# Kernel tuning notes

Measured on AMD Instinct MI355X. Metric: run time of the kernel, lower is better.

Reference implementation:

```python
import jax, jax.numpy as jnp
import numpy as np

BATCH = 16384
IN = 1024
OUT = 1024
SIGMA_MIN = 0.1
SIGMA_MAX = 1.0


def setup_inputs() -> dict:
    key = jax.random.key(0)
    k0, k1, k2, k3 = jax.random.split(key, 4)
    x = jax.random.normal(k0, (BATCH, IN), dtype=jnp.float32)
    # torch init: triu(randn) -> upper-triangular reflector banks
    U = jnp.triu(jax.random.normal(k1, (IN, IN), dtype=jnp.float32))
    V = jnp.triu(jax.random.normal(k2, (OUT, OUT), dtype=jnp.float32))
    p = 0.001 * jax.random.normal(k3, (min(IN, OUT),), dtype=jnp.float32)
    bias = jnp.zeros((OUT,), dtype=jnp.float32)
    return {"x": x, "U": U, "V": V, "p": p, "bias": bias}


def _hprod_step(x, u):
    # u has zeros in its first i entries (triu row i), so the full-vector
    # form equals torch's sliced Hprod on the last k = n - i columns.
    alpha = 2.0 * (x @ u) / jnp.dot(u, u)          # [bs]
    return x - alpha[:, None] * u[None, :], None   # rank-1 update


def reference(x, U, V, p, bias):
    r = (SIGMA_MAX - SIGMA_MIN) / 2.0
    sigma_mean = SIGMA_MIN + r
    # mask enforces torch slice semantics (entries below diag never used)
    Um = U * jnp.triu(jnp.ones_like(U))
    Vm = V * jnp.triu(jnp.ones_like(V))
    # Umultiply: reflectors i = 0 .. n_U-1 in order (sequential recurrence)
    x, _ = jax.lax.scan(_hprod_step, x, Um)
    # Sigma: diagonal scaling (square case IN == OUT)
    sigmas = 2.0 * r * (jax.nn.sigmoid(p) - 0.5) + sigma_mean
    x = x * sigmas[None, :]
    # Vmultiply: reflectors i = n_V-1 .. 0 (reverse order)
    x, _ = jax.lax.scan(_hprod_step, x, Vm[::-1])
    return x + bias
```

## Files before the change

kernel.cpp:

```cpp
#include <hip/hip_runtime.h>
#include <stdint.h>

typedef __attribute__((ext_vector_type(8))) short short8;
typedef __attribute__((ext_vector_type(4))) float f32x4;

#define NN 1024
#define NBATCH 16384
#define ME ((size_t)NN * NN)
#define AS1 (const __attribute__((address_space(1))) void*)
#define AS3 (__attribute__((address_space(3))) void*)

__device__ __forceinline__ unsigned short f32_to_bf16_rne(float f) {
  unsigned int u = __float_as_uint(f);
  unsigned int r = (u + 0x7fffu + ((u >> 16) & 1u)) >> 16;
  return (unsigned short)r;
}

__device__ __forceinline__ unsigned int pack2bf(float lo, float hi) {
  return (unsigned int)f32_to_bf16_rne(lo) | ((unsigned int)f32_to_bf16_rne(hi) << 16);
}

__device__ __forceinline__ void split_bf16(float x, unsigned short& h, unsigned short& l) {
  h = f32_to_bf16_rne(x);
  float hf = __uint_as_float((unsigned int)h << 16);
  l = f32_to_bf16_rne(x - hf);
}

__device__ __forceinline__ float allsum64(float x) {
  x += __int_as_float(__builtin_amdgcn_update_dpp(0, __float_as_int(x), 0xB1, 0xF, 0xF, true));
  x += __int_as_float(__builtin_amdgcn_update_dpp(0, __float_as_int(x), 0x4E, 0xF, 0xF, true));
  x += __int_as_float(__builtin_amdgcn_update_dpp(0, __float_as_int(x), 0x141, 0xF, 0xF, true));
  x += __int_as_float(__builtin_amdgcn_update_dpp(0, __float_as_int(x), 0x140, 0xF, 0xF, true));
#if __has_builtin(__builtin_amdgcn_permlane16_swap) && __has_builtin(__builtin_amdgcn_permlane32_swap)
  {
    auto r16 = __builtin_amdgcn_permlane16_swap(__float_as_uint(x), __float_as_uint(x), false, false);
    x = __uint_as_float(r16[0]) + __uint_as_float(r16[1]);
    auto r32 = __builtin_amdgcn_permlane32_swap(__float_as_uint(x), __float_as_uint(x), false, false);
    x = __uint_as_float(r32[0]) + __uint_as_float(r32[1]);
  }
#else
  x += __int_as_float(__builtin_amdgcn_ds_swizzle(__float_as_int(x), 0x401F));
  x += __shfl_xor(x, 32);
#endif
  return x;
}

__global__ __launch_bounds__(256) void prep_kernel(
    const float* __restrict__ U, const float* __restrict__ V,
    const float* __restrict__ p, float* __restrict__ tau_u,
    float* __restrict__ tau_v, float* __restrict__ sigmas) {
  int wave = threadIdx.x >> 6, lane = threadIdx.x & 63;
  int row = blockIdx.x * 4 + wave;
  if (row < 2048) {
    const float* u = (row < NN) ? (U + (size_t)row * NN) : (V + (size_t)(row - NN) * NN);
    float s = 0.f;
#pragma unroll
    for (int t = 0; t < 16; ++t) { float a = u[lane + (t << 6)]; s += a * a; }
    s = allsum64(s);
    if (lane == 0) {
      float tau = 2.0f / s;
      if (row < NN) tau_u[row] = tau;
      else tau_v[row - NN] = tau;
    }
  } else if (row < 2064) {
    int j = ((row - 2048) << 6) + lane;
    float pj = p[j];
    float sg = 1.0f / (1.0f + expf(-pj));
    sigmas[j] = 0.9f * (sg - 0.5f) + 0.55f;
  }
}

__global__ __launch_bounds__(256) void castx_kernel(
    const float* __restrict__ X, unsigned short* __restrict__ Xb) {
  const size_t n4 = (size_t)NBATCH * NN / 4;
  for (size_t i = (size_t)blockIdx.x * 256 + threadIdx.x; i < n4; i += (size_t)gridDim.x * 256) {
    float4 v = reinterpret_cast<const float4*>(X)[i];
    uint2 o;
    o.x = pack2bf(v.x, v.y);
    o.y = pack2bf(v.z, v.w);
    reinterpret_cast<uint2*>(Xb)[i] = o;
  }
}

__global__ __launch_bounds__(64) void gram_t8_kernel(
    const float* __restrict__ U, const float* __restrict__ V,
    const float* __restrict__ tau_u, const float* __restrict__ tau_v,
    float* __restrict__ T8all) {
  __shared__ float G[64];
  const int blk = blockIdx.x;
  const int lane = threadIdx.x;
  const float* bank;
  int rbase, rsign, st;
  if (blk < 128) { bank = U; rbase = 8 * blk; rsign = 1; st = 8 * blk; }
  else { int s = blk - 128; bank = V; rbase = 1023 - 8 * s; rsign = -1; st = 1016 - 8 * s; }

  if (lane < 28) {
    int j = 1, k = 0, t = lane;
    for (int jj = 1; jj < 8; ++jj) {
      int lo = jj * (jj - 1) / 2, hi = jj * (jj + 1) / 2;
      if (t >= lo && t < hi) { j = jj; k = t - lo; }
    }
    const float* rk = bank + (size_t)(rbase + rsign * k) * NN;
    const float* rj = bank + (size_t)(rbase + rsign * j) * NN;
    float acc = 0.f;
    for (int i = st >> 2; i < 256; ++i) {
      float4 a = *reinterpret_cast<const float4*>(rk + 4 * i);
      float4 b = *reinterpret_cast<const float4*>(rj + 4 * i);
      acc += a.x * b.x + a.y * b.y + a.z * b.z + a.w * b.w;
    }
    G[k * 8 + j] = acc;
  }
  __syncthreads();

  if (lane < 8) {
    float Tr[8];
#pragma unroll
    for (int j = 0; j < 8; ++j) Tr[j] = 0.f;
#pragma unroll
    for (int j = 0; j < 8; ++j) {
      int grow = rbase + rsign * j;
      float tj = (blk < 128) ? tau_u[grow] : tau_v[grow];
      float a = 0.f;
#pragma unroll
      for (int k = 0; k < 8; ++k) {
        if (k < j) a += Tr[k] * G[k * 8 + j];
      }
      Tr[j] = (lane == j) ? tj : (-tj * a);
    }
#pragma unroll
    for (int j = 0; j < 8; ++j) T8all[(size_t)blk * 64 + lane * 8 + j] = Tr[j];
  }
}

__global__ __launch_bounds__(256) void splity_kernel(
    const float* __restrict__ U, const float* __restrict__ V,
    unsigned short* __restrict__ Yhi, unsigned short* __restrict__ Ylo,
    unsigned short* __restrict__ YThi, unsigned short* __restrict__ YTlo) {
  __shared__ float ys[128][129];
  const int tid = threadIdx.x;
  const int c = blockIdx.x >> 3, et = blockIdx.x & 7;
  const int half = tid & 1;
  const int slot = tid >> 1;
  const int e0 = et << 7;
  const int grow = (c < 8) ? ((c << 7) + slot) : (1023 - ((c - 8) << 7) - slot);
  const float* src = ((c < 8) ? U : V) + (size_t)grow * NN + e0 + (half << 6);
#pragma unroll
  for (int i = 0; i < 16; ++i) {
    float4 v4 = *reinterpret_cast<const float4*>(src + (i << 2));
    const int kk = (half << 6) + (i << 2);
    ys[slot][kk + 0] = v4.x; ys[slot][kk + 1] = v4.y;
    ys[slot][kk + 2] = v4.z; ys[slot][kk + 3] = v4.w;
  }
  __syncthreads();
  {
    const size_t rbase = ((size_t)(c * 128 + slot)) * NN + e0 + (half << 6);
#pragma unroll
    for (int i = 0; i < 16; ++i) {
      const int kk = (half << 6) + (i << 2);
      ushort4 h4, l4;
      split_bf16(ys[slot][kk + 0], h4.x, l4.x);
      split_bf16(ys[slot][kk + 1], h4.y, l4.y);
      split_bf16(ys[slot][kk + 2], h4.z, l4.z);
      split_bf16(ys[slot][kk + 3], h4.w, l4.w);
      *reinterpret_cast<ushort4*>(&Yhi[rbase + (i << 2)]) = h4;
      *reinterpret_cast<ushort4*>(&Ylo[rbase + (i << 2)]) = l4;
    }
  }
  {
    const int e = slot;
    const size_t tbase = ((size_t)c * 1024 + e0 + e) * 128 + (half << 6);
#pragma unroll
    for (int i = 0; i < 16; ++i) {
      const int k0 = (half << 6) + (i << 2);
      ushort4 h4, l4;
      split_bf16(ys[k0 + 0][e], h4.x, l4.x);
      split_bf16(ys[k0 + 1][e], h4.y, l4.y);
      split_bf16(ys[k0 + 2][e], h4.z, l4.z);
      split_bf16(ys[k0 + 3][e], h4.w, l4.w);
      *reinterpret_cast<ushort4*>(&YThi[tbase + (i << 2)]) = h4;
      *reinterpret_cast<ushort4*>(&YTlo[tbase + (i << 2)]) = l4;
    }
  }
}

#define LDK 40
#define BM 128
#define BN 128
#define BK 32

__global__ __launch_bounds__(256) void gramt_kernel(
    const unsigned short* __restrict__ Yhi, const unsigned short* __restrict__ Ylo,
    float* __restrict__ Gp) {
  __shared__ unsigned short Hs[128 * LDK];
  __shared__ unsigned short Ls[128 * LDK];
  const int tid = threadIdx.x;
  const int lane = tid & 63, wave = tid >> 6;
  const int c = blockIdx.x >> 3, ks = blockIdx.x & 7;
  const int wm = wave & 1, wn = wave >> 1;
  const int srow = tid >> 1, scol = (tid & 1) << 4;
  const unsigned short* ph = Yhi + ((size_t)(c * 128 + srow)) * NN + ks * 128 + scol;
  const unsigned short* pl = Ylo + ((size_t)(c * 128 + srow)) * NN + ks * 128 + scol;

  f32x4 acc[4][4];
#pragma unroll
  for (int a = 0; a < 4; ++a)
#pragma unroll
    for (int b = 0; b < 4; ++b) acc[a][b] = 0.f;

  const int arow0 = wm * 64, brow0 = wn * 64;
  const int fr = lane & 15, kb = (lane >> 4) << 3;

#pragma unroll 1
  for (int kt = 0; kt < 4; ++kt) {
    __syncthreads();
    *reinterpret_cast<uint4*>(&Hs[srow * LDK + scol]) = *reinterpret_cast<const uint4*>(ph + kt * 32);
    *reinterpret_cast<uint4*>(&Hs[srow * LDK + scol + 8]) = *reinterpret_cast<const uint4*>(ph + kt * 32 + 8);
    *reinterpret_cast<uint4*>(&Ls[srow * LDK + scol]) = *reinterpret_cast<const uint4*>(pl + kt * 32);
    *reinterpret_cast<uint4*>(&Ls[srow * LDK + scol + 8]) = *reinterpret_cast<const uint4*>(pl + kt * 32 + 8);
    __syncthreads();
    short8 ah[4], al[4], bh[4], bl[4];
#pragma unroll
    for (int tr = 0; tr < 4; ++tr) {
      ah[tr] = *reinterpret_cast<const short8*>(&Hs[(arow0 + tr * 16 + fr) * LDK + kb]);
      al[tr] = *reinterpret_cast<const short8*>(&Ls[(arow0 + tr * 16 + fr) * LDK + kb]);
    }
#pragma unroll
    for (int tc = 0; tc < 4; ++tc) {
      bh[tc] = *reinterpret_cast<const short8*>(&Hs[(brow0 + tc * 16 + fr) * LDK + kb]);
      bl[tc] = *reinterpret_cast<const short8*>(&Ls[(brow0 + tc * 16 + fr) * LDK + kb]);
    }
#pragma unroll
    for (int tr = 0; tr < 4; ++tr)
#pragma unroll
      for (int tc = 0; tc < 4; ++tc) {
        acc[tr][tc] = __builtin_amdgcn_mfma_f32_16x16x32_bf16(ah[tr], bh[tc], acc[tr][tc], 0, 0, 0);
        acc[tr][tc] = __builtin_amdgcn_mfma_f32_16x16x32_bf16(ah[tr], bl[tc], acc[tr][tc], 0, 0, 0);
        acc[tr][tc] = __builtin_amdgcn_mfma_f32_16x16x32_bf16(al[tr], bh[tc], acc[tr][tc], 0, 0, 0);
      }
  }
  const int rq = (lane >> 4) << 2;
#pragma unroll
  for (int tc = 0; tc < 4; ++tc) {
    const int gc = brow0 + tc * 16 + fr;
#pragma unroll
    for (int tr = 0; tr < 4; ++tr) {
      const int gr = arow0 + tr * 16 + rq;
#pragma unroll
      for (int q = 0; q < 4; ++q)
        Gp[(((size_t)c * 8 + ks) * 128 + gr + q) * 128 + gc] = acc[tr][tc][q];
    }
  }
}

__global__ __launch_bounds__(256) void ttree_kernel(
    const float* __restrict__ Gp, const float* __restrict__ T8all,
    unsigned short* __restrict__ Thi, unsigned short* __restrict__ Tlo) {
  __shared__ float Ts[128 * 128];
  __shared__ float Gb[64 * 64];
  __shared__ float Xb[64 * 64];
  const int c = blockIdx.x, tid = threadIdx.x;
  for (int i = tid; i < 128 * 128; i += 256) Ts[i] = 0.f;
  __syncthreads();
  for (int i = tid; i < 1024; i += 256) {
    const int sb = i >> 6, ij = i & 63, r = ij >> 3, col = ij & 7;
    const int t8i = (c < 8) ? (16 * c + sb) : (128 + 16 * (c - 8) + sb);
    Ts[(8 * sb + r) * 128 + 8 * sb + col] = T8all[(size_t)t8i * 64 + ij];
  }
  __syncthreads();
  for (int b = 8; b <= 64; b <<= 1) {
    const int nm = 128 / (2 * b);
    for (int m = 0; m < nm; ++m) {
      const int a0 = 2 * b * m;
      for (int i = tid; i < b * b; i += 256) {
        const int r = i / b, cl = i % b;
        float s = 0.f;
#pragma unroll
        for (int sl = 0; sl < 8; ++sl)
          s += Gp[(((size_t)c * 8 + sl) * 128 + a0 + r) * 128 + a0 + b + cl];
        Gb[i] = s;
      }
      __syncthreads();
      for (int i = tid; i < b * b; i += 256) {
        const int r = i / b, cl = i % b;
        float s = 0.f;
        for (int k = 0; k <= cl; ++k)
          s += Gb[r * b + k] * Ts[(a0 + b + k) * 128 + a0 + b + cl];
        Xb[i] = s;
      }
      __syncthreads();
      for (int i = tid; i < b * b; i += 256) {
        const int r = i / b, cl = i % b;
        float s = 0.f;
        for (int k = r; k < b; ++k)
          s -= Ts[(a0 + r) * 128 + a0 + k] * Xb[k * b + cl];
        Ts[(a0 + r) * 128 + a0 + b + cl] = s;
      }
      __syncthreads();
    }
  }
  for (int i = tid; i < 128 * 128; i += 256) {
    unsigned short h, l;
    split_bf16(Ts[i], h, l);
    Thi[(size_t)c * 128 * 128 + i] = h;
    Tlo[(size_t)c * 128 * 128 + i] = l;
  }
}

__global__ __launch_bounds__(256) void zw_kernel(
    const unsigned short* __restrict__ Thi, const unsigned short* __restrict__ Tlo,
    const unsigned short* __restrict__ YThi, const unsigned short* __restrict__ YTlo,
    unsigned short* __restrict__ WThi, unsigned short* __restrict__ WTlo) {
  __shared__ unsigned short Xh[128 * LDK], Xl[128 * LDK];
  __shared__ unsigned short Wh[128 * LDK], Wl[128 * LDK];
  const int tid = threadIdx.x;
  const int lane = tid & 63, wave = tid >> 6;
  const int c = blockIdx.x >> 3, bn = blockIdx.x & 7;
  const int n0 = bn * 128;
  const int wm = wave & 1, wn = wave >> 1;
  const int srow = tid >> 1, scol = (tid & 1) << 4;
  const unsigned short* pxh = Thi + ((size_t)c * 128 + srow) * 128 + scol;
  const unsigned short* pxl = Tlo + ((size_t)c * 128 + srow) * 128 + scol;
  const unsigned short* pwh = YThi + ((size_t)c * 1024 + n0 + srow) * 128 + scol;
  const unsigned short* pwl = YTlo + ((size_t)c * 1024 + n0 + srow) * 128 + scol;

  f32x4 acc[4][4];
#pragma unroll
  for (int a = 0; a < 4; ++a)
#pragma unroll
    for (int b = 0; b < 4; ++b) acc[a][b] = 0.f;

  const int arow0 = wm * 64, brow0 = wn * 64;
  const int fr = lane & 15, kb = (lane >> 4) << 3;

#pragma unroll 1
  for (int kt = 0; kt < 4; ++kt) {
    __syncthreads();
    *reinterpret_cast<uint4*>(&Xh[srow * LDK + scol]) = *reinterpret_cast<const uint4*>(pxh + kt * 32);
    *reinterpret_cast<uint4*>(&Xh[srow * LDK + scol + 8]) = *reinterpret_cast<const uint4*>(pxh + kt * 32 + 8);
    *reinterpret_cast<uint4*>(&Xl[srow * LDK + scol]) = *reinterpret_cast<const uint4*>(pxl + kt * 32);
    *reinterpret_cast<uint4*>(&Xl[srow * LDK + scol + 8]) = *reinterpret_cast<const uint4*>(pxl + kt * 32 + 8);
    *reinterpret_cast<uint4*>(&Wh[srow * LDK + scol]) = *reinterpret_cast<const uint4*>(pwh + kt * 32);
    *reinterpret_cast<uint4*>(&Wh[srow * LDK + scol + 8]) = *reinterpret_cast<const uint4*>(pwh + kt * 32 + 8);
    *reinterpret_cast<uint4*>(&Wl[srow * LDK + scol]) = *reinterpret_cast<const uint4*>(pwl + kt * 32);
    *reinterpret_cast<uint4*>(&Wl[srow * LDK + scol + 8]) = *reinterpret_cast<const uint4*>(pwl + kt * 32 + 8);
    __syncthreads();
    short8 ah[4], al[4], bh[4], bl[4];
#pragma unroll
    for (int tr = 0; tr < 4; ++tr) {
      ah[tr] = *reinterpret_cast<const short8*>(&Xh[(arow0 + tr * 16 + fr) * LDK + kb]);
      al[tr] = *reinterpret_cast<const short8*>(&Xl[(arow0 + tr * 16 + fr) * LDK + kb]);
    }
#pragma unroll
    for (int tc = 0; tc < 4; ++tc) {
      bh[tc] = *reinterpret_cast<const short8*>(&Wh[(brow0 + tc * 16 + fr) * LDK + kb]);
      bl[tc] = *reinterpret_cast<const short8*>(&Wl[(brow0 + tc * 16 + fr) * LDK + kb]);
    }
#pragma unroll
    for (int tr = 0; tr < 4; ++tr)
#pragma unroll
      for (int tc = 0; tc < 4; ++tc) {
        acc[tr][tc] = __builtin_amdgcn_mfma_f32_16x16x32_bf16(ah[tr], bh[tc], acc[tr][tc], 0, 0, 0);
        acc[tr][tc] = __builtin_amdgcn_mfma_f32_16x16x32_bf16(ah[tr], bl[tc], acc[tr][tc], 0, 0, 0);
        acc[tr][tc] = __builtin_amdgcn_mfma_f32_16x16x32_bf16(al[tr], bh[tc], acc[tr][tc], 0, 0, 0);
      }
  }
  const int rq = (lane >> 4) << 2;
#pragma unroll
  for (int tc = 0; tc < 4; ++tc) {
    const int gc = brow0 + tc * 16 + fr;
#pragma unroll
    for (int tr = 0; tr < 4; ++tr) {
      const int gr = arow0 + tr * 16 + rq;
      ushort4 h4, l4;
      split_bf16(acc[tr][tc][0], h4.x, l4.x);
      split_bf16(acc[tr][tc][1], h4.y, l4.y);
      split_bf16(acc[tr][tc][2], h4.z, l4.z);
      split_bf16(acc[tr][tc][3], h4.w, l4.w);
      const size_t off = ((size_t)c * 1024 + n0 + gc) * 128 + gr;
      *reinterpret_cast<ushort4*>(&WThi[off]) = h4;
      *reinterpret_cast<ushort4*>(&WTlo[off]) = l4;
    }
  }
}

__global__ __launch_bounds__(256) void chainc_kernel(
    const unsigned short* __restrict__ YThi, const unsigned short* __restrict__ YTlo,
    const unsigned short* __restrict__ WThi, const unsigned short* __restrict__ WTlo,
    unsigned short* __restrict__ chains) {
  __shared__ unsigned short Xh[128 * LDK], Xl[128 * LDK];
  __shared__ unsigned short Wh[128 * LDK], Wl[128 * LDK];
  const int tid = threadIdx.x;
  const int lane = tid & 63, wave = tid >> 6;
  const int c = blockIdx.x >> 6, b6 = blockIdx.x & 63;
  const int bm = b6 & 7, bn = b6 >> 3;
  const int m0 = bm * 128, n0 = bn * 128;
  const int wm = wave & 1, wn = wave >> 1;
  const int srow = tid >> 1, scol = (tid & 1) << 4;
  const unsigned short* pxh = YThi + ((size_t)c * 1024 + m0 + srow) * 128 + scol;
  const unsigned short* pxl = YTlo + ((size_t)c * 1024 + m0 + srow) * 128 + scol;
  const unsigned short* pwh = WThi + ((size_t)c * 1024 + n0 + srow) * 128 + scol;
  const unsigned short* pwl = WTlo + ((size_t)c * 1024 + n0 + srow) * 128 + scol;

  f32x4 acc[4][4];
#pragma unroll
  for (int a = 0; a < 4; ++a)
#pragma unroll
    for (int b = 0; b < 4; ++b) acc[a][b] = 0.f;

  const int arow0 = wm * 64, brow0 = wn * 64;
  const int fr = lane & 15, kb = (lane >> 4) << 3;

#pragma unroll 1
  for (int kt = 0; kt < 4; ++kt) {
    __syncthreads();
    *reinterpret_cast<uint4*>(&Xh[srow * LDK + scol]) = *reinterpret_cast<const uint4*>(pxh + kt * 32);
    *reinterpret_cast<uint4*>(&Xh[srow * LDK + scol + 8]) = *reinterpret_cast<const uint4*>(pxh + kt * 32 + 8);
    *reinterpret_cast<uint4*>(&Xl[srow * LDK + scol]) = *reinterpret_cast<const uint4*>(pxl + kt * 32);
    *reinterpret_cast<uint4*>(&Xl[srow * LDK + scol + 8]) = *reinterpret_cast<const uint4*>(pxl + kt * 32 + 8);
    *reinterpret_cast<uint4*>(&Wh[srow * LDK + scol]) = *reinterpret_cast<const uint4*>(pwh + kt * 32);
    *reinterpret_cast<uint4*>(&Wh[srow * LDK + scol + 8]) = *reinterpret_cast<const uint4*>(pwh + kt * 32 + 8);
    *reinterpret_cast<uint4*>(&Wl[srow * LDK + scol]) = *reinterpret_cast<const uint4*>(pwl + kt * 32);
    *reinterpret_cast<uint4*>(&Wl[srow * LDK + scol + 8]) = *reinterpret_cast<const uint4*>(pwl + kt * 32 + 8);
    __syncthreads();
    short8 ah[4], al[4], bh[4], bl[4];
#pragma unroll
    for (int tr = 0; tr < 4; ++tr) {
      ah[tr] = *reinterpret_cast<const short8*>(&Xh[(arow0 + tr * 16 + fr) * LDK + kb]);
      al[tr] = *reinterpret_cast<const short8*>(&Xl[(arow0 + tr * 16 + fr) * LDK + kb]);
    }
#pragma unroll
    for (int tc = 0; tc < 4; ++tc) {
      bh[tc] = *reinterpret_cast<const short8*>(&Wh[(brow0 + tc * 16 + fr) * LDK + kb]);
      bl[tc] = *reinterpret_cast<const short8*>(&Wl[(brow0 + tc * 16 + fr) * LDK + kb]);
    }
#pragma unroll
    for (int tr = 0; tr < 4; ++tr)
#pragma unroll
      for (int tc = 0; tc < 4; ++tc) {
        acc[tr][tc] = __builtin_amdgcn_mfma_f32_16x16x32_bf16(ah[tr], bh[tc], acc[tr][tc], 0, 0, 0);
        acc[tr][tc] = __builtin_amdgcn_mfma_f32_16x16x32_bf16(ah[tr], bl[tc], acc[tr][tc], 0, 0, 0);
        acc[tr][tc] = __builtin_amdgcn_mfma_f32_16x16x32_bf16(al[tr], bh[tc], acc[tr][tc], 0, 0, 0);
      }
  }
  unsigned short* dst = chains + (size_t)c * ME;
  const int rq = (lane >> 4) << 2;
  if ((c & 1) == 0) {
#pragma unroll
    for (int tc = 0; tc < 4; ++tc) {
      const int gcg = n0 + brow0 + tc * 16 + fr;
#pragma unroll
      for (int tr = 0; tr < 4; ++tr) {
        const int grg = m0 + arow0 + tr * 16 + rq;
#pragma unroll
        for (int q = 0; q < 4; ++q) {
          const float val = ((grg + q) == gcg ? 1.0f : 0.0f) - acc[tr][tc][q];
          dst[(size_t)(grg + q) * NN + gcg] = f32_to_bf16_rne(val);
        }
      }
    }
  } else {
#pragma unroll
    for (int tc = 0; tc < 4; ++tc) {
      const int gcg = n0 + brow0 + tc * 16 + fr;
#pragma unroll
      for (int tr = 0; tr < 4; ++tr) {
        const int grg = m0 + arow0 + tr * 16 + rq;
        ushort4 pk;
        pk.x = f32_to_bf16_rne(((grg + 0) == gcg ? 1.0f : 0.0f) - acc[tr][tc][0]);
        pk.y = f32_to_bf16_rne(((grg + 1) == gcg ? 1.0f : 0.0f) - acc[tr][tc][1]);
        pk.z = f32_to_bf16_rne(((grg + 2) == gcg ? 1.0f : 0.0f) - acc[tr][tc][2]);
        pk.w = f32_to_bf16_rne(((grg + 3) == gcg ? 1.0f : 0.0f) - acc[tr][tc][3]);
        *reinterpret_cast<ushort4*>(&dst[(size_t)gcg * NN + grg]) = pk;
      }
    }
  }
}

__device__ __forceinline__ void cb_stage(
    const unsigned short* __restrict__ agbase, const unsigned short* __restrict__ bgbase,
    unsigned short* __restrict__ la, unsigned short* __restrict__ lb, int tid, int kt) {
#pragma unroll
  for (int i = 0; i < 2; ++i) {
    const int slot = tid + 256 * i;
    const int row = slot >> 2, s = slot & 3;
    __builtin_amdgcn_global_load_lds(
        AS1(agbase + (size_t)row * NN + kt * 32 + s * 8), AS3(la + row * 32 + s * 8), 16, 0, 0);
  }
#pragma unroll
  for (int i = 0; i < 2; ++i) {
    const int slot = tid + 256 * i;
    const int row = slot >> 2, s = slot & 3;
    __builtin_amdgcn_global_load_lds(
        AS1(bgbase + (size_t)row * NN + kt * 32 + s * 8), AS3(lb + row * 32 + s * 8), 16, 0, 0);
  }
}

__device__ __forceinline__ void cb_compute(
    const unsigned short* __restrict__ As, const unsigned short* __restrict__ Bs,
    f32x4 acc[4][4], int arow0, int brow0, int fr, int kb) {
  short8 af[4], bf[4];
#pragma unroll
  for (int tr = 0; tr < 4; ++tr)
    af[tr] = *reinterpret_cast<const short8*>(&As[(arow0 + tr * 16 + fr) * 32 + kb]);
#pragma unroll
  for (int tc = 0; tc < 4; ++tc)
    bf[tc] = *reinterpret_cast<const short8*>(&Bs[(brow0 + tc * 16 + fr) * 32 + kb]);
#pragma unroll
  for (int tr = 0; tr < 4; ++tr)
#pragma unroll
    for (int tc = 0; tc < 4; ++tc)
      acc[tr][tc] = __builtin_amdgcn_mfma_f32_16x16x32_bf16(af[tr], bf[tc], acc[tr][tc], 0, 0, 0);
}

__device__ __forceinline__ void compose_body(
    const unsigned short* __restrict__ Xb, const unsigned short* __restrict__ Wb,
    unsigned short* __restrict__ Op, const float* __restrict__ sig, int b, bool tstore) {
  __shared__ unsigned short As[3][BM * 32];
  __shared__ unsigned short Bs[3][BN * 32];
  const int tid = threadIdx.x;
  const int lane = tid & 63, wave = tid >> 6;
  const int bm = b & 7, bn = b >> 3;
  const int m0 = bm * BM, n0 = bn * BN;
  const int wm = wave & 1, wn = wave >> 1;
  const int arow0 = wm * 64, brow0 = wn * 64;
  const int fr = lane & 15, kb = (lane >> 4) << 3;

  f32x4 acc[4][4];
#pragma unroll
  for (int a = 0; a < 4; ++a)
#pragma unroll
    for (int bb = 0; bb < 4; ++bb) acc[a][bb] = 0.f;

  const unsigned short* agbase = Xb + (size_t)m0 * NN;
  const unsigned short* bgbase = Wb + (size_t)n0 * NN;

  cb_stage(agbase, bgbase, &As[0][0], &Bs[0][0], tid, 0);
  cb_stage(agbase, bgbase, &As[1][0], &Bs[1][0], tid, 1);
#pragma unroll 1
  for (int kt = 0; kt < 31; ++kt) {
    asm volatile("s_waitcnt vmcnt(4)" ::: "memory");
    __builtin_amdgcn_s_barrier();
    __builtin_amdgcn_sched_barrier(0);
    if (kt + 2 < 32) {
      const int nb = (kt + 2) % 3;
      cb_stage(agbase, bgbase, &As[nb][0], &Bs[nb][0], tid, kt + 2);
    }
    cb_compute(&As[kt % 3][0], &Bs[kt % 3][0], acc, arow0, brow0, fr, kb);
  }
  asm volatile("s_waitcnt vmcnt(0)" ::: "memory");
  __builtin_amdgcn_s_barrier();
  __builtin_amdgcn_sched_barrier(0);
  cb_compute(&As[1][0], &Bs[1][0], acc, arow0, brow0, fr, kb);

  const int rq = (lane >> 4) << 2;
  if (!tstore) {
#pragma unroll
    for (int tc = 0; tc < 4; ++tc) {
      const int gc = n0 + brow0 + tc * 16 + fr;
      const float s = sig ? sig[gc] : 1.0f;
#pragma unroll
      for (int tr = 0; tr < 4; ++tr) {
        const int gr = m0 + arow0 + tr * 16 + rq;
#pragma unroll
        for (int q = 0; q < 4; ++q) {
          Op[(size_t)(gr + q) * NN + gc] = f32_to_bf16_rne(acc[tr][tc][q] * s);
        }
      }
    }
  } else {
#pragma unroll
    for (int tc = 0; tc < 4; ++tc) {
      const int gc = n0 + brow0 + tc * 16 + fr;
#pragma unroll
      for (int tr = 0; tr < 4; ++tr) {
        const int gr = m0 + arow0 + tr * 16 + rq;
        ushort4 pk;
        pk.x = f32_to_bf16_rne(acc[tr][tc][0]);
        pk.y = f32_to_bf16_rne(acc[tr][tc][1]);
        pk.z = f32_to_bf16_rne(acc[tr][tc][2]);
        pk.w = f32_to_bf16_rne(acc[tr][tc][3]);
        *reinterpret_cast<ushort4*>(&Op[(size_t)gc * NN + gr]) = pk;
      }
    }
  }
}

__global__ __launch_bounds__(256) void composeL1_kernel(
    const unsigned short* __restrict__ ch, unsigned short* __restrict__ P) {
  const int sub = blockIdx.x >> 6, b = blockIdx.x & 63;
  const int i = sub & 3;
  const unsigned short* x = ch + (size_t)((sub < 4 ? 0 : 8) + 2 * i) * ME;
  compose_body(x, x + ME, P + (size_t)sub * ME, nullptr, b, (i & 1) != 0);
}

__global__ __launch_bounds__(256) void composeL2_kernel(
    const unsigned short* __restrict__ P, unsigned short* __restrict__ Q) {
  const int sub = blockIdx.x >> 6, b = blockIdx.x & 63;
  compose_body(P + (size_t)(2 * sub) * ME, P + (size_t)(2 * sub + 1) * ME,
               Q + (size_t)sub * ME, nullptr, b, (sub & 1) != 0);
}

__global__ __launch_bounds__(256) void composeL3_kernel(
    const unsigned short* __restrict__ Q, const float* __restrict__ sigmas,
    unsigned short* __restrict__ F) {
  const int sub = blockIdx.x >> 6, b = blockIdx.x & 63;
  if (sub == 0) compose_body(Q, Q + ME, F, sigmas, b, false);
  else compose_body(Q + 2 * ME, Q + 3 * ME, F + ME, nullptr, b, true);
}

__global__ __launch_bounds__(256) void composeL4_kernel(
    const unsigned short* __restrict__ F, unsigned short* __restrict__ Mt) {
  compose_body(F + ME, F, Mt, nullptr, blockIdx.x, false);
}

__global__ __launch_bounds__(512) void gemm256_kernel(
    const unsigned short* __restrict__ Xb, const unsigned short* __restrict__ Mt,
    const float* __restrict__ bias, float* __restrict__ Out) {
  __shared__ unsigned short As[3][256 * 32];
  __shared__ unsigned short Bs[3][128 * 32];
  const int tid = threadIdx.x;
  const int lane = tid & 63, wave = tid >> 6;
  const int bm = blockIdx.x & 63, bn = blockIdx.x >> 6;
  const int m0 = bm * 256, n0 = bn * 128;
  const int wm = wave & 3, wn = wave >> 2;
  const int arow0 = wm * 64, brow0 = wn * 64;
  const int fr = lane & 15, kb = (lane >> 4) << 3;

  f32x4 acc[4][4];
#pragma unroll
  for (int a = 0; a < 4; ++a)
#pragma unroll
    for (int b = 0; b < 4; ++b) acc[a][b] = 0.f;

  const unsigned short* agbase = Xb + (size_t)m0 * NN;
  const unsigned short* bgbase = Mt + (size_t)n0 * NN;

#define G256_STAGE(B, KT)                                                        \
  {                                                                              \
    _Pragma("unroll")                                                            \
    for (int i = 0; i < 2; ++i) {                                                \
      const int slot = tid + 512 * i;                                            \
      const int row = slot >> 2, s = slot & 3;                                   \
      __builtin_amdgcn_global_load_lds(                                          \
          AS1(agbase + (size_t)row * NN + (KT) * 32 + s * 8),                    \
          AS3(&As[B][row * 32 + s * 8]), 16, 0, 0);                              \
    }                                                                            \
    {                                                                            \
      const int row = tid >> 2, s = tid & 3;                                     \
      __builtin_amdgcn_global_load_lds(                                          \
          AS1(bgbase + (size_t)row * NN + (KT) * 32 + s * 8),                    \
          AS3(&Bs[B][row * 32 + s * 8]), 16, 0, 0);                              \
    }                                                                            \
  }

#define G256_CMP(B)                                                              \
  {                                                                              \
    short8 af[4], bf4[4];                                                        \
    _Pragma("unroll")                                                            \
    for (int tr = 0; tr < 4; ++tr)                                               \
      af[tr] = *reinterpret_cast<const short8*>(&As[B][(arow0 + tr * 16 + fr) * 32 + kb]); \
    _Pragma("unroll")                                                            \
    for (int tc = 0; tc < 4; ++tc)                                               \
      bf4[tc] = *reinterpret_cast<const short8*>(&Bs[B][(brow0 + tc * 16 + fr) * 32 + kb]); \
    _Pragma("unroll")                                                            \
    for (int tr = 0; tr < 4; ++tr)                                               \
      _Pragma("unroll")                                                          \
      for (int tc = 0; tc < 4; ++tc)                                             \
        acc[tr][tc] = __builtin_amdgcn_mfma_f32_16x16x32_bf16(af[tr], bf4[tc], acc[tr][tc], 0, 0, 0); \
  }

  G256_STAGE(0, 0)
  G256_STAGE(1, 1)
#pragma unroll 1
  for (int kt = 0; kt < 31; ++kt) {
    asm volatile("s_waitcnt vmcnt(3)" ::: "memory");
    __builtin_amdgcn_s_barrier();
    __builtin_amdgcn_sched_barrier(0);
    if (kt + 2 < 32) {
      const int nb = (kt + 2) % 3;
      G256_STAGE(nb, kt + 2)
    }
    G256_CMP(kt % 3)
  }
  asm volatile("s_waitcnt vmcnt(0)" ::: "memory");
  __builtin_amdgcn_s_barrier();
  __builtin_amdgcn_sched_barrier(0);
  G256_CMP(1)
#undef G256_STAGE
#undef G256_CMP

  const int rq = (lane >> 4) << 2;
#pragma unroll
  for (int tc = 0; tc < 4; ++tc) {
    const int gc = n0 + brow0 + tc * 16 + fr;
    const float bv = bias[gc];
#pragma unroll
    for (int tr = 0; tr < 4; ++tr) {
      const int gr = m0 + arow0 + tr * 16 + rq;
#pragma unroll
      for (int q = 0; q < 4; ++q) {
        Out[(size_t)(gr + q) * NN + gc] = acc[tr][tc][q] + bv;
      }
    }
  }
}

__global__ __launch_bounds__(256) void gemm_fb_kernel(
    const float* __restrict__ X, const unsigned short* __restrict__ Mt,
    const float* __restrict__ bias, float* __restrict__ Out) {
  __shared__ float Af[2][BM * 32];
  __shared__ unsigned short Bsl[2][BN * 32];
  const int tid = threadIdx.x;
  const int lane = tid & 63, wave = tid >> 6;
  const int bm = blockIdx.x & 127;
  const int bn = blockIdx.x >> 7;
  const int m0 = bm * BM, n0 = bn * BN;
  const int wm = wave & 1, wn = wave >> 1;
  const int arow0 = wm * 64, brow0 = wn * 64;
  const int fr = lane & 15, kb = (lane >> 4) << 3;

  f32x4 acc[4][4];
#pragma unroll
  for (int a = 0; a < 4; ++a)
#pragma unroll
    for (int b = 0; b < 4; ++b) acc[a][b] = 0.f;

  const float* agbase = X + (size_t)m0 * NN;
  const unsigned short* bgbase = Mt + (size_t)n0 * NN;

#define FB_STAGE(PB, KT)                                                        \
  {                                                                             \
    _Pragma("unroll")                                                           \
    for (int i = 0; i < 4; ++i) {                                               \
      const int slot = tid + 256 * i;                                           \
      const int row = slot >> 3, s = slot & 7;                                  \
      __builtin_amdgcn_global_load_lds(                                         \
          AS1(agbase + (size_t)row * NN + (KT) * 32 + s * 4),                   \
          AS3(&Af[PB][row * 32 + s * 4]), 16, 0, 0);                            \
    }                                                                           \
    _Pragma("unroll")                                                           \
    for (int i = 0; i < 2; ++i) {                                               \
      const int slot = tid + 256 * i;                                           \
      const int row = slot >> 2, s = slot & 3;                                  \
      __builtin_amdgcn_global_load_lds(                                         \
          AS1(bgbase + (size_t)row * NN + (KT) * 32 + s * 8),                   \
          AS3(&Bsl[PB][row * 32 + s * 8]), 16, 0, 0);                           \
    }                                                                           \
  }

  FB_STAGE(0, 0)
  int pb = 0;
#pragma unroll 1
  for (int kt = 0; kt < 32; ++kt) {
    __syncthreads();
    if (kt + 1 < 32) FB_STAGE(pb ^ 1, kt + 1)
    {
      short8 af[4], bf[4];
      const int c0 = kb >> 2;
#pragma unroll
      for (int tr = 0; tr < 4; ++tr) {
        const int row = arow0 + tr * 16 + fr;
        const f32x4 a0 = *reinterpret_cast<const f32x4*>(&Af[pb][row * 32 + c0 * 4]);
        const f32x4 a1 = *reinterpret_cast<const f32x4*>(&Af[pb][row * 32 + (c0 + 1) * 4]);
        uint4 w;
        w.x = pack2bf(a0[0], a0[1]); w.y = pack2bf(a0[2], a0[3]);
        w.z = pack2bf(a1[0], a1[1]); w.w = pack2bf(a1[2], a1[3]);
        af[tr] = *reinterpret_cast<const short8*>(&w);
      }
#pragma unroll
      for (int tc = 0; tc < 4; ++tc) {
        const int row = brow0 + tc * 16 + fr;
        bf[tc] = *reinterpret_cast<const short8*>(&Bsl[pb][row * 32 + kb]);
      }
#pragma unroll
      for (int tr = 0; tr < 4; ++tr)
#pragma unroll
        for (int tc = 0; tc < 4; ++tc)
          acc[tr][tc] = __builtin_amdgcn_mfma_f32_16x16x32_bf16(af[tr], bf[tc], acc[tr][tc], 0, 0, 0);
    }
    pb ^= 1;
  }
#undef FB_STAGE

  const int rq = (lane >> 4) << 2;
#pragma unroll
  for (int tc = 0; tc < 4; ++tc) {
    const int gc = n0 + brow0 + tc * 16 + fr;
    const float bv = bias[gc];
#pragma unroll
    for (int tr = 0; tr < 4; ++tr) {
      const int gr = m0 + arow0 + tr * 16 + rq;
#pragma unroll
      for (int q = 0; q < 4; ++q) {
        Out[(size_t)(gr + q) * NN + gc] = acc[tr][tc][q] + bv;
      }
    }
  }
}

extern "C" void kernel_launch(void* const* d_in, const int* in_sizes, int n_in,
                              void* d_out, int out_size, void* d_ws, size_t ws_size,
                              hipStream_t stream) {
  const float* x = (const float*)d_in[0];
  const float* U = (const float*)d_in[1];
  const float* V = (const float*)d_in[2];
  const float* p = (const float*)d_in[3];
  const float* bias = (const float*)d_in[4];
  float* out = (float*)d_out;

  char* ws = (char*)d_ws;
  float* tau_u = (float*)(ws);
  float* tau_v = (float*)(ws + 4096);
  float* sigmas = (float*)(ws + 8192);
  float* T8all = (float*)(ws + 16384);
  unsigned short* Mt = (unsigned short*)(ws + 81920);

  const size_t XB_OFF = 4u * 1024 * 1024;
  const size_t XB_BYTES = (size_t)NBATCH * NN * 2;
  const bool fast = ws_size >= XB_OFF + XB_BYTES;
  unsigned short* Xb = (unsigned short*)(ws + XB_OFF);

  unsigned short* sc = (unsigned short*)d_out;
  unsigned short* chains = sc;
  unsigned short* P = sc + 16 * ME;
  unsigned short* Q = sc + 24 * ME;
  unsigned short* F = sc + 28 * ME;
  unsigned short* YThi = sc + 16 * ME;
  unsigned short* YTlo = sc + 18 * ME;
  unsigned short* WThi = sc + 20 * ME;
  unsigned short* WTlo = sc + 22 * ME;
  unsigned short* Yhi = sc + 24 * ME;
  unsigned short* Ylo = sc + 26 * ME;
  float* Gp = (float*)(sc + 28 * ME);
  unsigned short* Thi = sc + 24 * ME;
  unsigned short* Tlo = Thi + 262144;

  prep_kernel<<<516, 256, 0, stream>>>(U, V, p, tau_u, tau_v, sigmas);
  if (fast) castx_kernel<<<2048, 256, 0, stream>>>(x, Xb);
  gram_t8_kernel<<<256, 64, 0, stream>>>(U, V, tau_u, tau_v, T8all);
  splity_kernel<<<128, 256, 0, stream>>>(U, V, Yhi, Ylo, YThi, YTlo);
  gramt_kernel<<<128, 256, 0, stream>>>(Yhi, Ylo, Gp);
  ttree_kernel<<<16, 256, 0, stream>>>(Gp, T8all, Thi, Tlo);
  zw_kernel<<<128, 256, 0, stream>>>(Thi, Tlo, YThi, YTlo, WThi, WTlo);
  chainc_kernel<<<1024, 256, 0, stream>>>(YThi, YTlo, WThi, WTlo, chains);
  composeL1_kernel<<<512, 256, 0, stream>>>(chains, P);
  composeL2_kernel<<<256, 256, 0, stream>>>(P, Q);
  composeL3_kernel<<<128, 256, 0, stream>>>(Q, sigmas, F);
  composeL4_kernel<<<64, 256, 0, stream>>>(F, Mt);
  if (fast) gemm256_kernel<<<512, 512, 0, stream>>>(Xb, Mt, bias, out);
  else gemm_fb_kernel<<<1024, 256, 0, stream>>>(x, Mt, bias, out);
}
```

Before: 335.5 us.

## Split triangular T-tree build into parallel per-level merge kernels

Replaces the single 16-block kernel that serially built each block-reflector T factor with a sequence of kernels. One kernel pre-sums the Gram partials and initializes T, one kernel per tree level runs the independent merges across blocks, and a final kernel does the bf16 split with vectorized stores. This removes redundant global re-reads of partial sums and the serialized per-block merge loop, at the cost of extra launches and a trip through global memory between levels.

```diff
diff --git a/kernel.cpp b/kernel.cpp
--- a/kernel.cpp
+++ b/kernel.cpp
@@ -252,57 +252,81 @@
   }
 }
 
-__global__ __launch_bounds__(256) void ttree_kernel(
+__global__ __launch_bounds__(256) void gsum_tinit_kernel(
     const float* __restrict__ Gp, const float* __restrict__ T8all,
-    unsigned short* __restrict__ Thi, unsigned short* __restrict__ Tlo) {
-  __shared__ float Ts[128 * 128];
-  __shared__ float Gb[64 * 64];
-  __shared__ float Xb[64 * 64];
-  const int c = blockIdx.x, tid = threadIdx.x;
-  for (int i = tid; i < 128 * 128; i += 256) Ts[i] = 0.f;
+    float* __restrict__ G, float* __restrict__ Tg) {
+  const int bid = blockIdx.x;
+  if (bid < 1024) {
+    const size_t i = (size_t)bid * 256 + threadIdx.x;
+    const size_t c = i >> 14, rc = i & 16383;
+    float s = 0.f;
+#pragma unroll
+    for (int sl = 0; sl < 8; ++sl)
+      s += Gp[(c * 8 + sl) * 16384 + rc];
+    G[i] = s;
+  } else {
+    const size_t base = ((size_t)(bid - 1024) * 256 + threadIdx.x) * 16;
+#pragma unroll 1
+    for (int e = 0; e < 16; ++e) {
+      const size_t i = base + e;
+      const int c = (int)(i >> 14), rc = (int)(i & 16383);
+      const int r = rc >> 7, cl = rc & 127;
+      float v = 0.f;
+      if ((r >> 3) == (cl >> 3)) {
+        const int sb = r >> 3;
+        const int t8i = (c < 8) ? (16 * c + sb) : (128 + 16 * (c - 8) + sb);
+        v = T8all[(size_t)t8i * 64 + (r & 7) * 8 + (cl & 7)];
+      }
+      Tg[i] = v;
+    }
+  }
+}
+
+template <int B>
+__global__ __launch_bounds__(256) void tmerge_kernel(
+    const float* __restrict__ G, float* __restrict__ Tg) {
+  __shared__ float T1s[B * B], T2s[B * B], Gs[B * B], Xs[B * B];
+  const int nm = 128 / (2 * B);
+  const int c = blockIdx.x / nm, m = blockIdx.x % nm;
+  const int a0 = 2 * B * m;
+  const int tid = threadIdx.x;
+  float* Tc = Tg + (size_t)c * 16384;
+  for (int i = tid; i < B * B; i += 256) {
+    const int r = i / B, cl = i % B;
+    T1s[i] = Tc[(a0 + r) * 128 + a0 + cl];
+    T2s[i] = Tc[(a0 + B + r) * 128 + a0 + B + cl];
+    Gs[i] = G[((size_t)c * 128 + a0 + r) * 128 + a0 + B + cl];
+  }
   __syncthreads();
-  for (int i = tid; i < 1024; i += 256) {
-    const int sb = i >> 6, ij = i & 63, r = ij >> 3, col = ij & 7;
-    const int t8i = (c < 8) ? (16 * c + sb) : (128 + 16 * (c - 8) + sb);
-    Ts[(8 * sb + r) * 128 + 8 * sb + col] = T8all[(size_t)t8i * 64 + ij];
+  for (int i = tid; i < B * B; i += 256) {
+    const int r = i / B, cl = i % B;
+    float s = 0.f;
+    for (int k = 0; k <= cl; ++k) s += Gs[r * B + k] * T2s[k * B + cl];
+    Xs[i] = s;
   }
   __syncthreads();
-  for (int b = 8; b <= 64; b <<= 1) {
-    const int nm = 128 / (2 * b);
-    for (int m = 0; m < nm; ++m) {
-      const int a0 = 2 * b * m;
-      for (int i = tid; i < b * b; i += 256) {
-        const int r = i / b, cl = i % b;
-        float s = 0.f;
-#pragma unroll
-        for (int sl = 0; sl < 8; ++sl)
-          s += Gp[(((size_t)c * 8 + sl) * 128 + a0 + r) * 128 + a0 + b + cl];
-        Gb[i] = s;
-      }
-      __syncthreads();
-      for (int i = tid; i < b * b; i += 256) {
-        const int r = i / b, cl = i % b;
-        float s = 0.f;
-        for (int k = 0; k <= cl; ++k)
-          s += Gb[r * b + k] * Ts[(a0 + b + k) * 128 + a0 + b + cl];
-        Xb[i] = s;
-      }
-      __syncthreads();
-      for (int i = tid; i < b * b; i += 256) {
-        const int r = i / b, cl = i % b;
-        float s = 0.f;
-        for (int k = r; k < b; ++k)
-          s -= Ts[(a0 + r) * 128 + a0 + k] * Xb[k * b + cl];
-        Ts[(a0 + r) * 128 + a0 + b + cl] = s;
-      }
-      __syncthreads();
-    }
-  }
-  for (int i = tid; i < 128 * 128; i += 256) {
-    unsigned short h, l;
-    split_bf16(Ts[i], h, l);
-    Thi[(size_t)c * 128 * 128 + i] = h;
-    Tlo[(size_t)c * 128 * 128 + i] = l;
+  for (int i = tid; i < B * B; i += 256) {
+    const int r = i / B, cl = i % B;
+    float s = 0.f;
+    for (int k = r; k < B; ++k) s -= T1s[r * B + k] * Xs[k * B + cl];
+    Tc[(a0 + r) * 128 + a0 + B + cl] = s;
+  }
+}
+
+__global__ __launch_bounds__(256) void tsplit_kernel(
+    const float* __restrict__ Tg, unsigned short* __restrict__ Thi,
+    unsigned short* __restrict__ Tlo) {
+  const size_t i0 = ((size_t)blockIdx.x * 256 + threadIdx.x) * 16;
+#pragma unroll
+  for (int v = 0; v < 4; ++v) {
+    float4 t = *reinterpret_cast<const float4*>(Tg + i0 + 4 * v);
+    ushort4 h4, l4;
+    split_bf16(t.x, h4.x, l4.x);
+    split_bf16(t.y, h4.y, l4.y);
+    split_bf16(t.z, h4.z, l4.z);
+    split_bf16(t.w, h4.w, l4.w);
+    *reinterpret_cast<ushort4*>(&Thi[i0 + 4 * v]) = h4;
+    *reinterpret_cast<ushort4*>(&Tlo[i0 + 4 * v]) = l4;
   }
 }
 
@@ -832,6 +856,8 @@
   unsigned short* Yhi = sc + 24 * ME;
   unsigned short* Ylo = sc + 26 * ME;
   float* Gp = (float*)(sc + 28 * ME);
+  float* G = (float*)sc;
+  float* Tg = (float*)(sc + ME);
   unsigned short* Thi = sc + 24 * ME;
   unsigned short* Tlo = Thi + 262144;
 
@@ -840,7 +866,12 @@
   gram_t8_kernel<<<256, 64, 0, stream>>>(U, V, tau_u, tau_v, T8all);
   splity_kernel<<<128, 256, 0, stream>>>(U, V, Yhi, Ylo, YThi, YTlo);
   gramt_kernel<<<128, 256, 0, stream>>>(Yhi, Ylo, Gp);
-  ttree_kernel<<<16, 256, 0, stream>>>(Gp, T8all, Thi, Tlo);
+  gsum_tinit_kernel<<<1088, 256, 0, stream>>>(Gp, T8all, G, Tg);
+  tmerge_kernel<8><<<128, 256, 0, stream>>>(G, Tg);
+  tmerge_kernel<16><<<64, 256, 0, stream>>>(G, Tg);
+  tmerge_kernel<32><<<32, 256, 0, stream>>>(G, Tg);
+  tmerge_kernel<64><<<16, 256, 0, stream>>>(G, Tg);
+  tsplit_kernel<<<64, 256, 0, stream>>>(Tg, Thi, Tlo);
   zw_kernel<<<128, 256, 0, stream>>>(Thi, Tlo, YThi, YTlo, WThi, WTlo);
   chainc_kernel<<<1024, 256, 0, stream>>>(YThi, YTlo, WThi, WTlo, chains);
   composeL1_kernel<<<512, 256, 0, stream>>>(chains, P);
```

After: 325.2 us. -3.1%, faster.
